# Kernel optimization log

Hardware: AMD Instinct MI355X
Metric: run time of the kernel (lower is better)

## Reference

```python
import jax, jax.numpy as jnp
import numpy as np

B, T, D = 2, 2048, 2048
H = 16
NOPE, ROPE = 128, 64
Q_HEAD = NOPE + ROPE            # 192
Q_LORA = H * Q_HEAD // 4        # 768
KV_RANK = 512
V_DIM = 128
EPS = 1e-6


def setup_inputs() -> dict:
    key = jax.random.key(0)
    ks = jax.random.split(key, 8)
    s = lambda k, shape: jax.random.normal(k, shape, dtype=jnp.float32) * (1.0 / np.sqrt(shape[0]))
    return {
        "hidden_states": jax.random.normal(ks[0], (B, T, D), dtype=jnp.float32),
        "positions": jnp.broadcast_to(jnp.arange(T, dtype=jnp.int64 if jax.config.jax_enable_x64 else jnp.int32), (B, T)),
        "w_qa": s(ks[1], (D, Q_LORA)),
        "g_qa": jnp.ones((Q_LORA,), jnp.float32),
        "w_qb": s(ks[2], (Q_LORA, H * Q_HEAD)),
        "w_kva": s(ks[3], (D, KV_RANK + ROPE)),
        "g_kva": jnp.ones((KV_RANK,), jnp.float32),
        "w_kvb": s(ks[4], (KV_RANK, H * (NOPE + V_DIM))),
        "w_o": s(ks[5], (H * V_DIM, D)),
    }


def _rms(x, g):
    return x * jax.lax.rsqrt(jnp.mean(x * x, axis=-1, keepdims=True) + EPS) * g


def _rotate_half(x):
    h = x.shape[-1] // 2
    return jnp.concatenate([-x[..., h:], x[..., :h]], axis=-1)


def _rope_tables(n):
    inv_freq = 1.0 / (10000.0 ** (jnp.arange(0, ROPE, 2, dtype=jnp.float32) / ROPE))
    freqs = jnp.arange(n, dtype=jnp.float32)[:, None] * inv_freq[None, :]
    emb = jnp.concatenate([freqs, freqs], axis=-1)  # [n, ROPE]
    return jnp.cos(emb), jnp.sin(emb)


def reference(hidden_states, positions, w_qa, g_qa, w_qb, w_kva, g_kva, w_kvb, w_o):
    Bq, Tq, _ = hidden_states.shape
    # Q: low-rank down-proj + RMSNorm + up-proj
    q = _rms(hidden_states @ w_qa, g_qa) @ w_qb
    q = q.reshape(Bq, Tq, H, Q_HEAD)
    q_nope, q_rope = q[..., :NOPE], q[..., NOPE:]
    # KV compression (prefill: no past cache, S == T)
    kvc = hidden_states @ w_kva
    new_c_kv = _rms(kvc[..., :KV_RANK], g_kva)     # [B,S,rank]
    new_k_rope = kvc[..., KV_RANK:]                # [B,S,ROPE]
    S = new_c_kv.shape[1]
    kv = (new_c_kv @ w_kvb).reshape(Bq, S, H, NOPE + V_DIM)
    k_nope, v = kv[..., :NOPE], kv[..., NOPE:]
    # Decoupled RoPE on the rope sub-dimension only
    cos_full, sin_full = _rope_tables(S)
    cos_q = cos_full[positions][:, :, None, :]     # [B,T,1,ROPE]
    sin_q = sin_full[positions][:, :, None, :]
    q_rope = q_rope * cos_q + _rotate_half(q_rope) * sin_q
    cos_k = cos_full[None, :, :]                   # [1,S,ROPE] (all_positions = arange(S))
    sin_k = sin_full[None, :, :]
    k_rope = new_k_rope * cos_k + _rotate_half(new_k_rope) * sin_k  # [B,S,ROPE], shared across heads
    # Assemble full q/k, attention
    q_full = jnp.concatenate([q_nope, q_rope], axis=-1).transpose(0, 2, 1, 3)  # [B,H,T,192]
    k_full = jnp.concatenate(
        [k_nope, jnp.broadcast_to(k_rope[:, :, None, :], (Bq, S, H, ROPE))], axis=-1
    ).transpose(0, 2, 1, 3)                                                     # [B,H,S,192]
    v = v.transpose(0, 2, 1, 3)                                                 # [B,H,S,Vd]
    scale = Q_HEAD ** -0.5
    attn = jnp.einsum("bhtd,bhsd->bhts", q_full, k_full) * scale
    row = jnp.arange(Tq)[:, None]
    col = jnp.arange(S)[None, :]
    attn = jnp.where(col > row + (S - Tq), -jnp.inf, attn)
    attn = jax.nn.softmax(attn, axis=-1)
    out = jnp.einsum("bhts,bhsd->bhtd", attn, v)
    out = out.transpose(0, 2, 1, 3).reshape(Bq, Tq, H * V_DIM)
    output = out @ w_o
    return output, new_c_kv, new_k_rope
```

## Files before the change

### kernel.cpp

```cpp
#include <hip/hip_runtime.h>
#include <stdint.h>

typedef unsigned short ushort_t;
typedef ushort_t u16x8 __attribute__((ext_vector_type(8)));
typedef short s16x8 __attribute__((ext_vector_type(8)));
typedef float f32x4 __attribute__((ext_vector_type(4)));

#define B_ 2
#define T_ 2048
#define D_ 2048
#define H_ 16
#define NOPE_ 128
#define ROPE_ 64
#define QHEAD_ 192
#define QLORA_ 768
#define KVRANK_ 512
#define VDIM_ 128
#define MROWS (B_*T_)
#define QKVW 1408

#define MAGIC_F32  0x3F800000u
#define MAGIC_BF16 0x3F803F80u

#define QK_SCALE2 0.10411754851533622f
#define DEFER_THR 11.5415603271117f

__device__ __forceinline__ float bf2f(ushort_t u) {
    return __uint_as_float(((uint32_t)u) << 16);
}
__device__ __forceinline__ ushort_t f2bf(float f) {
    uint32_t x = __float_as_uint(f);
    x += 0x7fffu + ((x >> 16) & 1u);
    return (ushort_t)(x >> 16);
}

__device__ __forceinline__ void async_ld16(const ushort_t* g, ushort_t* l) {
    __builtin_amdgcn_global_load_lds(
        (const __attribute__((address_space(1))) void*)g,
        (__attribute__((address_space(3))) void*)l, 16, 0, 0);
}

__device__ __forceinline__ void xcd_tile(int& m0, int& n0) {
    const int nx = gridDim.x;
    const int nwg = nx * gridDim.y;
    int lin = (int)blockIdx.y * nx + (int)blockIdx.x;
    lin = (lin & 7) * (nwg >> 3) + (lin >> 3);
    n0 = (lin % nx) * 128;
    m0 = (lin / nx) * 128;
}

__launch_bounds__(256)
__global__ void gemm_mfma(const ushort_t* __restrict__ A,
                          const ushort_t* __restrict__ BT,
                          float* __restrict__ C, int M, int N, int K) {
    __shared__ ushort_t As[128 * 32];
    __shared__ ushort_t Bs[128 * 32];

    const int tid = threadIdx.x;
    const int lane = tid & 63;
    const int n16 = lane & 15, quad = lane >> 4;
    int m0, n0;
    xcd_tile(m0, n0);
    const int w = tid >> 6;
    const int wm = (w & 1) * 64, wn = (w >> 1) * 64;

    f32x4 acc[4][4];
#pragma unroll
    for (int i = 0; i < 4; i++)
#pragma unroll
        for (int j = 0; j < 4; j++) acc[i][j] = (f32x4){0.f, 0.f, 0.f, 0.f};

    const int wbase = tid & ~63;
    for (int kt = 0; kt < K; kt += 32) {
        __syncthreads();
#pragma unroll
        for (int iss = 0; iss < 2; iss++) {
            const int chunk = iss * 256 + tid;
            const int row = chunk >> 2, col = (chunk & 3) * 8;
            const int lbase = (iss * 256 + wbase) * 8;
            async_ld16(A + (long)(m0 + row) * K + kt + col, &As[lbase]);
            async_ld16(BT + (long)(n0 + row) * K + kt + col, &Bs[lbase]);
        }
        __syncthreads();

        s16x8 af[4], bf[4];
#pragma unroll
        for (int i = 0; i < 4; i++) {
            af[i] = *(const s16x8*)&As[(wm + i * 16 + n16) * 32 + quad * 8];
            bf[i] = *(const s16x8*)&Bs[(wn + i * 16 + n16) * 32 + quad * 8];
        }
#pragma unroll
        for (int i = 0; i < 4; i++)
#pragma unroll
            for (int j = 0; j < 4; j++)
                acc[i][j] = __builtin_amdgcn_mfma_f32_16x16x32_bf16(af[i], bf[j], acc[i][j], 0, 0, 0);
    }

#pragma unroll
    for (int i = 0; i < 4; i++) {
        const long mrow = m0 + wm + i * 16 + quad * 4;
#pragma unroll
        for (int j = 0; j < 4; j++) {
            const int nc = n0 + wn + j * 16 + n16;
#pragma unroll
            for (int r = 0; r < 4; r++)
                C[(mrow + r) * N + nc] = acc[i][j][r];
        }
    }
}

__launch_bounds__(256)
__global__ void gemm_mfma_h(const ushort_t* __restrict__ A,
                            const ushort_t* __restrict__ BT,
                            ushort_t* __restrict__ C, int M, int N, int K) {
    __shared__ ushort_t As[128 * 32];
    __shared__ ushort_t Bs[128 * 32];

    const int tid = threadIdx.x;
    const int lane = tid & 63;
    const int n16 = lane & 15, quad = lane >> 4;
    int m0, n0;
    xcd_tile(m0, n0);
    const int w = tid >> 6;
    const int wm = (w & 1) * 64, wn = (w >> 1) * 64;

    f32x4 acc[4][4];
#pragma unroll
    for (int i = 0; i < 4; i++)
#pragma unroll
        for (int j = 0; j < 4; j++) acc[i][j] = (f32x4){0.f, 0.f, 0.f, 0.f};

    const int wbase = tid & ~63;
    for (int kt = 0; kt < K; kt += 32) {
        __syncthreads();
#pragma unroll
        for (int iss = 0; iss < 2; iss++) {
            const int chunk = iss * 256 + tid;
            const int row = chunk >> 2, col = (chunk & 3) * 8;
            const int lbase = (iss * 256 + wbase) * 8;
            async_ld16(A + (long)(m0 + row) * K + kt + col, &As[lbase]);
            async_ld16(BT + (long)(n0 + row) * K + kt + col, &Bs[lbase]);
        }
        __syncthreads();

        s16x8 af[4], bf[4];
#pragma unroll
        for (int i = 0; i < 4; i++) {
            af[i] = *(const s16x8*)&As[(wm + i * 16 + n16) * 32 + quad * 8];
            bf[i] = *(const s16x8*)&Bs[(wn + i * 16 + n16) * 32 + quad * 8];
        }
#pragma unroll
        for (int i = 0; i < 4; i++)
#pragma unroll
            for (int j = 0; j < 4; j++)
                acc[i][j] = __builtin_amdgcn_mfma_f32_16x16x32_bf16(af[i], bf[j], acc[i][j], 0, 0, 0);
    }

#pragma unroll
    for (int i = 0; i < 4; i++) {
        const long mrow = m0 + wm + i * 16 + quad * 4;
#pragma unroll
        for (int j = 0; j < 4; j++) {
            const int nc = n0 + wn + j * 16 + n16;
#pragma unroll
            for (int r = 0; r < 4; r++)
                C[(mrow + r) * N + nc] = f2bf(acc[i][j][r]);
        }
    }
}

__launch_bounds__(256)
__global__ void gemm_out_k(const uint32_t* __restrict__ probe,
                           const ushort_t* __restrict__ A,
                           const ushort_t* __restrict__ BT,
                           float* __restrict__ Cf, ushort_t* __restrict__ Ch,
                           int M, int N, int K) {
    __shared__ ushort_t As[128 * 32];
    __shared__ ushort_t Bs[128 * 32];

    const bool isf = (*probe == MAGIC_F32);
    const int tid = threadIdx.x;
    const int lane = tid & 63;
    const int n16 = lane & 15, quad = lane >> 4;
    int m0, n0;
    xcd_tile(m0, n0);
    const int w = tid >> 6;
    const int wm = (w & 1) * 64, wn = (w >> 1) * 64;

    f32x4 acc[4][4];
#pragma unroll
    for (int i = 0; i < 4; i++)
#pragma unroll
        for (int j = 0; j < 4; j++) acc[i][j] = (f32x4){0.f, 0.f, 0.f, 0.f};

    const int wbase = tid & ~63;
    for (int kt = 0; kt < K; kt += 32) {
        __syncthreads();
#pragma unroll
        for (int iss = 0; iss < 2; iss++) {
            const int chunk = iss * 256 + tid;
            const int row = chunk >> 2, col = (chunk & 3) * 8;
            const int lbase = (iss * 256 + wbase) * 8;
            async_ld16(A + (long)(m0 + row) * K + kt + col, &As[lbase]);
            async_ld16(BT + (long)(n0 + row) * K + kt + col, &Bs[lbase]);
        }
        __syncthreads();

        s16x8 af[4], bf[4];
#pragma unroll
        for (int i = 0; i < 4; i++) {
            af[i] = *(const s16x8*)&As[(wm + i * 16 + n16) * 32 + quad * 8];
            bf[i] = *(const s16x8*)&Bs[(wn + i * 16 + n16) * 32 + quad * 8];
        }
#pragma unroll
        for (int i = 0; i < 4; i++)
#pragma unroll
            for (int j = 0; j < 4; j++)
                acc[i][j] = __builtin_amdgcn_mfma_f32_16x16x32_bf16(af[i], bf[j], acc[i][j], 0, 0, 0);
    }

#pragma unroll
    for (int i = 0; i < 4; i++) {
        const long mrow = m0 + wm + i * 16 + quad * 4;
#pragma unroll
        for (int j = 0; j < 4; j++) {
            const int nc = n0 + wn + j * 16 + n16;
            if (isf) {
#pragma unroll
                for (int r = 0; r < 4; r++)
                    Cf[(mrow + r) * N + nc] = acc[i][j][r];
            } else {
#pragma unroll
                for (int r = 0; r < 4; r++)
                    Ch[(mrow + r) * N + nc] = f2bf(acc[i][j][r]);
            }
        }
    }
}

__launch_bounds__(256)
__global__ void gemm_kv_k(const ushort_t* __restrict__ A,
                          const ushort_t* __restrict__ BT,
                          ushort_t* __restrict__ kvK,
                          ushort_t* __restrict__ vTm,
                          int M, int N, int K) {
    __shared__ ushort_t As[128 * 32];
    __shared__ ushort_t Bs[128 * 32];

    const int tid = threadIdx.x;
    const int lane = tid & 63;
    const int n16 = lane & 15, quad = lane >> 4;
    int m0, n0;
    xcd_tile(m0, n0);
    const int w = tid >> 6;
    const int wm = (w & 1) * 64, wn = (w >> 1) * 64;

    f32x4 acc[4][4];
#pragma unroll
    for (int i = 0; i < 4; i++)
#pragma unroll
        for (int j = 0; j < 4; j++) acc[i][j] = (f32x4){0.f, 0.f, 0.f, 0.f};

    const int wbase = tid & ~63;
    for (int kt = 0; kt < K; kt += 32) {
        __syncthreads();
#pragma unroll
        for (int iss = 0; iss < 2; iss++) {
            const int chunk = iss * 256 + tid;
            const int row = chunk >> 2, col = (chunk & 3) * 8;
            const int lbase = (iss * 256 + wbase) * 8;
            async_ld16(A + (long)(m0 + row) * K + kt + col, &As[lbase]);
            async_ld16(BT + (long)(n0 + row) * K + kt + col, &Bs[lbase]);
        }
        __syncthreads();

        s16x8 af[4], bf[4];
#pragma unroll
        for (int i = 0; i < 4; i++) {
            af[i] = *(const s16x8*)&As[(wm + i * 16 + n16) * 32 + quad * 8];
            bf[i] = *(const s16x8*)&Bs[(wn + i * 16 + n16) * 32 + quad * 8];
        }
#pragma unroll
        for (int i = 0; i < 4; i++)
#pragma unroll
            for (int j = 0; j < 4; j++)
                acc[i][j] = __builtin_amdgcn_mfma_f32_16x16x32_bf16(af[i], bf[j], acc[i][j], 0, 0, 0);
    }

    const bool isV = (n0 & 128) != 0;
    if (!isV) {
#pragma unroll
        for (int i = 0; i < 4; i++) {
            const long mrowb = m0 + wm + i * 16 + quad * 4;
#pragma unroll
            for (int j = 0; j < 4; j++) {
                const int nc = n0 + wn + j * 16 + n16;
                const int hh = nc >> 8, dd = nc & 127;
#pragma unroll
                for (int r = 0; r < 4; r++)
                    kvK[(mrowb + r) * (H_ * NOPE_) + hh * NOPE_ + dd] = f2bf(acc[i][j][r]);
            }
        }
    } else {
        __syncthreads();
        ushort_t* tb = (w < 2) ? &As[w * 1152] : &Bs[(w - 2) * 1152];
        const int hh  = (n0 + wn) >> 8;
        const long bb = (long)((m0 + wm) >> 11);
        const int ssb = (m0 + wm) & (T_ - 1);
        const int ddb = (n0 + wn) & 127;
        const int ddr = lane >> 2;
        const int c0  = (lane & 3) * 16;
#pragma unroll
        for (int j = 0; j < 4; j++) {
#pragma unroll
            for (int i = 0; i < 4; i++)
#pragma unroll
                for (int r = 0; r < 4; r++)
                    tb[n16 * 72 + i * 16 + quad * 4 + r] = f2bf(acc[i][j][r]);
            u16x8 v0 = *(const u16x8*)&tb[ddr * 72 + c0];
            u16x8 v1 = *(const u16x8*)&tb[ddr * 72 + c0 + 8];
            ushort_t* dstp = vTm + ((bb * H_ + hh) * VDIM_ + ddb + j * 16 + ddr) * (long)T_ + ssb + c0;
            *(u16x8*)dstp = v0;
            *(u16x8*)(dstp + 8) = v1;
        }
    }
}

__launch_bounds__(256)
__global__ void cvt_trans_k(const uint32_t* __restrict__ probe,
                            const float* __restrict__ srcf,
                            const ushort_t* __restrict__ srch,
                            ushort_t* __restrict__ dst,
                            int K, int N, int NP, float scl) {
    const bool isf = (*probe == MAGIC_F32);
    __shared__ float tile[32][33];
    const int kb = blockIdx.y * 32, nb = blockIdx.x * 32;
    const int tx = threadIdx.x & 31, ty = threadIdx.x >> 5;
#pragma unroll
    for (int i = 0; i < 32; i += 8) {
        const int n = nb + tx;
        const long idx = (long)(kb + ty + i) * N + n;
        tile[ty + i][tx] = (n < N) ? (isf ? srcf[idx] : bf2f(srch[idx])) : 0.f;
    }
    __syncthreads();
#pragma unroll
    for (int i = 0; i < 32; i += 8) {
        const int n = nb + ty + i;
        if (n < NP) dst[(long)n * K + kb + tx] = f2bf(tile[tx][ty + i] * scl);
    }
}

__launch_bounds__(256)
__global__ void cvt_copy_k(const uint32_t* __restrict__ probe,
                           const float* __restrict__ srcf,
                           const ushort_t* __restrict__ srch,
                           ushort_t* __restrict__ dst, long n) {
    const bool isf = (*probe == MAGIC_F32);
    const long i = ((long)blockIdx.x * 256 + threadIdx.x) * 8;
    if (i + 8 <= n) {
        u16x8 o;
        if (isf) {
            float4 a = *(const float4*)(srcf + i);
            float4 b = *(const float4*)(srcf + i + 4);
            o[0]=f2bf(a.x); o[1]=f2bf(a.y); o[2]=f2bf(a.z); o[3]=f2bf(a.w);
            o[4]=f2bf(b.x); o[5]=f2bf(b.y); o[6]=f2bf(b.z); o[7]=f2bf(b.w);
        } else {
            o = *(const u16x8*)(srch + i);
        }
        *(u16x8*)(dst + i) = o;
    }
}

__launch_bounds__(256)
__global__ void rms12rope_k(const uint32_t* __restrict__ probe,
                            const float* __restrict__ qkv,
                            const float* __restrict__ g1f, const ushort_t* __restrict__ g1h,
                            const float* __restrict__ g2f, const ushort_t* __restrict__ g2h,
                            ushort_t* __restrict__ qln,
                            float* __restrict__ ockf, ushort_t* __restrict__ ockh,
                            ushort_t* __restrict__ ckv_i,
                            float* __restrict__ okrf, ushort_t* __restrict__ okrh,
                            ushort_t* __restrict__ krope_rot) {
    const bool isf = (*probe == MAGIC_F32);
    const int row = blockIdx.x;
    const int tid = threadIdx.x;
    const float* ir = qkv + (long)row * QKVW;

    float s1 = 0.f, s2 = 0.f;
    for (int c = tid; c < QLORA_; c += 256) { float x = ir[c]; s1 += x * x; }
    for (int c = tid; c < KVRANK_; c += 256) { float x = ir[QLORA_ + c]; s2 += x * x; }
    __shared__ float r1[256], r2[256];
    r1[tid] = s1; r2[tid] = s2;
    __syncthreads();
    for (int s = 128; s > 0; s >>= 1) {
        if (tid < s) { r1[tid] += r1[tid + s]; r2[tid] += r2[tid + s]; }
        __syncthreads();
    }
    const float inv1 = rsqrtf(r1[0] / (float)QLORA_ + 1e-6f);
    const float inv2 = rsqrtf(r2[0] / (float)KVRANK_ + 1e-6f);

    for (int c = tid; c < QLORA_; c += 256)
        qln[(long)row * QLORA_ + c] = f2bf(ir[c] * inv1 * (isf ? g1f[c] : bf2f(g1h[c])));
    for (int c = tid; c < KVRANK_; c += 256) {
        const float v = ir[QLORA_ + c] * inv2 * (isf ? g2f[c] : bf2f(g2h[c]));
        if (isf) ockf[(long)row * KVRANK_ + c] = v;
        else     ockh[(long)row * KVRANK_ + c] = f2bf(v);
        ckv_i[(long)row * KVRANK_ + c] = f2bf(v);
    }

    if (tid < 64) {
        const int lane = tid;
        const int t = row & (T_ - 1);
        const float x = ir[QLORA_ + KVRANK_ + lane];
        const float other = ir[QLORA_ + KVRANK_ + (lane ^ 32)];
        const int fi = lane & 31;
        const float inv_freq = exp2f((float)fi * (-13.287712379549449f / 32.f));
        const float ang = (float)t * inv_freq;
        float sn, cs;
        sincosf(ang, &sn, &cs);
        const float rot = (lane < 32) ? -other : other;
        if (isf) okrf[(long)row * ROPE_ + lane] = x;
        else     okrh[(long)row * ROPE_ + lane] = f2bf(x);
        krope_rot[(long)row * ROPE_ + lane] = f2bf(x * cs + rot * sn);
    }
}

#define BQ 64
#define BK 64
#define PSTR 68

__launch_bounds__(256, 2)
__global__ void attn_mfma_k(const ushort_t* __restrict__ q,
                            const ushort_t* __restrict__ kvK,
                            const ushort_t* __restrict__ vTm,
                            const ushort_t* __restrict__ krope,
                            ushort_t* __restrict__ attn_out) {
    __shared__ ushort_t ks[2][BK * 192];
    __shared__ ushort_t ps[4][16][PSTR];

    const int tid = threadIdx.x;
    const int w = tid >> 6, lane = tid & 63;
    const int n16 = lane & 15, quad = lane >> 4;

    const int L = (int)blockIdx.x;
    const int slot = L >> 3;
    const int bhg = slot >> 5;
    const int qts = slot & 31;
    const int bh = (L & 7) | (bhg << 3);
    const int qt = (bhg & 1) ? (31 - qts) : qts;
    const int h = bh & (H_ - 1), b = bh >> 4;

    const int q0 = qt * BQ;
    const int qw = q0 + w * 16;

    s16x8 qf[6];
    {
        const ushort_t* qrow = q + (long)(b * T_ + qw + n16) * (H_ * QHEAD_) + h * QHEAD_;
#pragma unroll
        for (int c = 0; c < 6; c++)
            qf[c] = *(const s16x8*)(qrow + c * 32 + quad * 8);
    }
    {
        const int t = qw + n16;
#pragma unroll
        for (int j = 0; j < 8; j++) {
            const int d = quad * 8 + j;
            const float inv_freq = exp2f((float)d * (-13.287712379549449f / 32.f));
            float sn, cs;
            sincosf((float)t * inv_freq, &sn, &cs);
            const float x0 = bf2f((ushort_t)qf[4][j]);
            const float x1 = bf2f((ushort_t)qf[5][j]);
            qf[4][j] = (short)f2bf(x0 * cs - x1 * sn);
            qf[5][j] = (short)f2bf(x1 * cs + x0 * sn);
        }
    }

    s16x8 kones;
#pragma unroll
    for (int j = 0; j < 8; j++) kones[j] = (short)0x3F80;

    f32x4 O[8];
#pragma unroll
    for (int f = 0; f < 8; f++) O[f] = (f32x4){0.f, 0.f, 0.f, 0.f};
    float mrow[4], lrow[4];
#pragma unroll
    for (int r = 0; r < 4; r++) { mrow[r] = -3.0e38f; lrow[r] = 0.f; }

    const int ntiles = qt + 1;

    const ushort_t* spb[6];  int sstr[6];
#pragma unroll
    for (int i = 0; i < 6; i++) {
        const int off = w * 6144 + i * 1024 + lane * 16;
        const int row = off / 384;
        const int c16 = (off % 384) >> 4;
        const int csrc = c16 ^ (row & 7);
        if (csrc < 16) {
            spb[i] = kvK + (long)(b * T_ + row) * (H_ * NOPE_) + h * NOPE_ + csrc * 8;
            sstr[i] = H_ * NOPE_;
        } else {
            spb[i] = krope + (long)(b * T_ + row) * ROPE_ + (csrc - 16) * 8;
            sstr[i] = ROPE_;
        }
    }

    const ushort_t* vbase = vTm + ((long)bh * VDIM_ + n16) * T_ + quad * 8;
    const int r7 = n16 & 7;

#pragma unroll
    for (int i = 0; i < 6; i++)
        async_ld16(spb[i], &ks[0][w * 3072 + i * 512]);

    int cur = 0;
    for (int kt = 0; kt < ntiles; kt++) {
        const int s0 = kt * BK;
        const int sn = (kt + 1 < ntiles ? kt + 1 : kt) * BK;

        s16x8 vb[2][8];
#pragma unroll
        for (int kc = 0; kc < 2; kc++)
#pragma unroll
            for (int vt = 0; vt < 8; vt++)
                vb[kc][vt] = *(const s16x8*)(vbase + (long)(vt * 16) * T_ + s0 + kc * 32);
        __builtin_amdgcn_sched_barrier(0);

        asm volatile("s_waitcnt vmcnt(16)" ::: "memory");
        __builtin_amdgcn_s_barrier();
        __builtin_amdgcn_sched_barrier(0);

#pragma unroll
        for (int i = 0; i < 6; i++)
            async_ld16(spb[i] + (long)sn * sstr[i], &ks[cur ^ 1][w * 3072 + i * 512]);
        __builtin_amdgcn_sched_barrier(0);

        const ushort_t* kb = &ks[cur][0];
        f32x4 Sc[4];
        __builtin_amdgcn_s_setprio(1);
#pragma unroll
        for (int st = 0; st < 4; st++) {
            Sc[st] = (f32x4){0.f, 0.f, 0.f, 0.f};
            const int row = st * 16 + n16;
            const int rbase = row * 192;
#pragma unroll
            for (int c = 0; c < 4; c++) {
                s16x8 bfr = *(const s16x8*)&kb[rbase + (((4 * c + quad) ^ r7) << 3)];
                Sc[st] = __builtin_amdgcn_mfma_f32_16x16x32_bf16(qf[c], bfr, Sc[st], 0, 0, 0);
            }
#pragma unroll
            for (int c2 = 0; c2 < 2; c2++) {
                s16x8 bfr = *(const s16x8*)&kb[rbase + (((16 + 4 * c2 + quad) ^ r7) << 3)];
                Sc[st] = __builtin_amdgcn_mfma_f32_16x16x32_bf16(qf[4 + c2], bfr, Sc[st], 0, 0, 0);
            }
        }
        __builtin_amdgcn_s_setprio(0);

        const bool diag = (s0 + BK > q0);
        float Sv[4][4];
#pragma unroll
        for (int st = 0; st < 4; st++) {
            const int sg = s0 + st * 16 + n16;
#pragma unroll
            for (int r = 0; r < 4; r++) {
                float v = Sc[st][r];
                if (diag && sg > qw + quad * 4 + r) v = -3.0e38f;
                Sv[st][r] = v;
            }
        }

        float rmx[4];
#pragma unroll
        for (int r = 0; r < 4; r++)
            rmx[r] = fmaxf(fmaxf(Sv[0][r], Sv[1][r]), fmaxf(Sv[2][r], Sv[3][r]));

        bool ok = true;
#pragma unroll
        for (int r = 0; r < 4; r++) ok = ok && (rmx[r] <= mrow[r] + DEFER_THR);
        if (!__all(ok)) {
            float mnew[4], alpha[4];
#pragma unroll
            for (int r = 0; r < 4; r++) {
                float mx = rmx[r];
#pragma unroll
                for (int off = 8; off > 0; off >>= 1)
                    mx = fmaxf(mx, __shfl_xor(mx, off, 64));
                mnew[r] = fmaxf(mrow[r], mx);
                alpha[r] = exp2f(mrow[r] - mnew[r]);
                mrow[r] = mnew[r];
                lrow[r] *= alpha[r];
            }
#pragma unroll
            for (int f = 0; f < 8; f++)
#pragma unroll
                for (int r = 0; r < 4; r++) O[f][r] *= alpha[r];
        }

#pragma unroll
        for (int st = 0; st < 4; st++)
#pragma unroll
            for (int r = 0; r < 4; r++)
                ps[w][quad * 4 + r][st * 16 + n16] = f2bf(exp2f(Sv[st][r] - mrow[r]));

        asm volatile("s_waitcnt vmcnt(6)" ::: "memory");
        __builtin_amdgcn_sched_barrier(0);

        f32x4 sacc = (f32x4){0.f, 0.f, 0.f, 0.f};
        __builtin_amdgcn_s_setprio(1);
#pragma unroll
        for (int kc = 0; kc < 2; kc++) {
            s16x8 afr = *(const s16x8*)&ps[w][n16][kc * 32 + quad * 8];
            sacc = __builtin_amdgcn_mfma_f32_16x16x32_bf16(afr, kones, sacc, 0, 0, 0);
#pragma unroll
            for (int vt = 0; vt < 8; vt++)
                O[vt] = __builtin_amdgcn_mfma_f32_16x16x32_bf16(afr, vb[kc][vt], O[vt], 0, 0, 0);
        }
        __builtin_amdgcn_s_setprio(0);
#pragma unroll
        for (int r = 0; r < 4; r++) lrow[r] += sacc[r];

        cur ^= 1;
    }

    float linv[4];
#pragma unroll
    for (int r = 0; r < 4; r++) linv[r] = 1.f / lrow[r];
    ushort_t* obase = attn_out + (long)(b * T_ + qw) * (H_ * VDIM_) + h * VDIM_;
#pragma unroll
    for (int vt = 0; vt < 8; vt++)
#pragma unroll
        for (int r = 0; r < 4; r++)
            obase[(long)(quad * 4 + r) * (H_ * VDIM_) + vt * 16 + n16] =
                f2bf(O[vt][r] * linv[r]);
}

extern "C" void kernel_launch(void* const* d_in, const int* in_sizes, int n_in,
                              void* d_out, int out_size, void* d_ws, size_t ws_size,
                              hipStream_t stream) {
    const uint32_t* probe = (const uint32_t*)d_in[3];

    char* ws = (char*)d_ws;
    ushort_t* q      = (ushort_t*)ws;
    ushort_t* hs_b   = (ushort_t*)ws;
    ushort_t* woT    = (ushort_t*)ws;
    ushort_t* kvK    = (ushort_t*)(ws + 25165824);
    ushort_t* vTm    = (ushort_t*)(ws + 41943040);
    float*    qkv    = (float*)(ws + 25165824);
    ushort_t* wqaT   = (ushort_t*)(ws + 48234496);
    ushort_t* wkvaT  = (ushort_t*)(ws + 51380224);
    ushort_t* wqbT   = (ushort_t*)(ws + 48234496);
    ushort_t* attn_i = (ushort_t*)(ws + 58720256);
    ushort_t* ckv_i  = (ushort_t*)(ws + 58720256);
    ushort_t* qln    = (ushort_t*)(ws + 62914560);
    ushort_t* wkvbT  = (ushort_t*)(ws + 69206016);
    ushort_t* krope  = (ushort_t*)(ws + 76283904 - 786432);

    const float* hs_f  = (const float*)d_in[0];
    const float* wqa_f = (const float*)d_in[2];
    const float* gqa_f = (const float*)d_in[3];
    const float* wqb_f = (const float*)d_in[4];
    const float* wkva_f= (const float*)d_in[5];
    const float* gkva_f= (const float*)d_in[6];
    const float* wkvb_f= (const float*)d_in[7];
    const float* wo_f  = (const float*)d_in[8];
    float* oy_f  = (float*)d_out;
    float* ock_f = oy_f + (long)MROWS * D_;
    float* okr_f = ock_f + (long)MROWS * KVRANK_;

    const ushort_t* hs_h  = (const ushort_t*)d_in[0];
    const ushort_t* wqa_h = (const ushort_t*)d_in[2];
    const ushort_t* gqa_h = (const ushort_t*)d_in[3];
    const ushort_t* wqb_h = (const ushort_t*)d_in[4];
    const ushort_t* wkva_h= (const ushort_t*)d_in[5];
    const ushort_t* gkva_h= (const ushort_t*)d_in[6];
    const ushort_t* wkvb_h= (const ushort_t*)d_in[7];
    const ushort_t* wo_h  = (const ushort_t*)d_in[8];
    ushort_t* oy_h  = (ushort_t*)d_out;
    ushort_t* ock_h = oy_h + (long)MROWS * D_;
    ushort_t* okr_h = ock_h + (long)MROWS * KVRANK_;

    const dim3 blk(256);

    cvt_copy_k<<<4096, blk, 0, stream>>>(probe, hs_f, hs_h, hs_b, (long)MROWS * D_);
    cvt_trans_k<<<dim3(24, 64), blk, 0, stream>>>(probe, wqa_f, wqa_h, wqaT, D_, QLORA_, QLORA_, 1.f);
    cvt_trans_k<<<dim3(20, 64), blk, 0, stream>>>(probe, wkva_f, wkva_h, wkvaT, D_, KVRANK_ + ROPE_, 640, 1.f);

    gemm_mfma<<<dim3(QKVW / 128, MROWS / 128), blk, 0, stream>>>(hs_b, wqaT, qkv, MROWS, QKVW, D_);

    rms12rope_k<<<MROWS, blk, 0, stream>>>(probe, qkv, gqa_f, gqa_h, gkva_f, gkva_h,
                                           qln, ock_f, ock_h, ckv_i, okr_f, okr_h, krope);

    cvt_trans_k<<<dim3(96, 24), blk, 0, stream>>>(probe, wqb_f, wqb_h, wqbT, QLORA_, H_ * QHEAD_, H_ * QHEAD_, QK_SCALE2);
    gemm_mfma_h<<<dim3((H_ * QHEAD_) / 128, MROWS / 128), blk, 0, stream>>>(qln, wqbT, q, MROWS, H_ * QHEAD_, QLORA_);

    cvt_trans_k<<<dim3(128, 16), blk, 0, stream>>>(probe, wkvb_f, wkvb_h, wkvbT, KVRANK_, H_ * 256, H_ * 256, 1.f);
    gemm_kv_k<<<dim3((H_ * 256) / 128, MROWS / 128), blk, 0, stream>>>(ckv_i, wkvbT, kvK, vTm, MROWS, H_ * 256, KVRANK_);

    attn_mfma_k<<<dim3(B_ * H_ * (T_ / BQ)), blk, 0, stream>>>(q, kvK, vTm, krope, attn_i);

    cvt_trans_k<<<dim3(64, 64), blk, 0, stream>>>(probe, wo_f, wo_h, woT, H_ * VDIM_, D_, D_, 1.f);
    gemm_out_k<<<dim3(D_ / 128, MROWS / 128), blk, 0, stream>>>(probe, attn_i, woT, oy_f, oy_h, MROWS, D_, H_ * VDIM_);
}
```

Measured before the change: 506.8 us.

## Widen GEMM K-tile to 64 and software-pipeline QK scores in attention

All four GEMM kernels now stage 64-wide K slices into shared memory instead of 32, halving the number of barrier pairs per output tile at the cost of doubled LDS use. The attention kernel is restructured so the QK score MFMAs for the next key tile are computed while the current tile's softmax and PV run, with K prefetch moved two tiles ahead. This is meant to hide LDS and global-load latency behind MFMA work, but it adds register pressure from the extra score accumulators.

```diff
diff --git a/kernel.cpp b/kernel.cpp
--- a/kernel.cpp
+++ b/kernel.cpp
@@ -49,12 +49,40 @@
     m0 = (lin / nx) * 128;
 }
 
+#define GEMM_STAGE64(As, Bs)                                                   \
+    __syncthreads();                                                           \
+    _Pragma("unroll")                                                          \
+    for (int iss = 0; iss < 4; iss++) {                                        \
+        const int chunk = iss * 256 + tid;                                     \
+        const int row = chunk >> 3, col = (chunk & 7) * 8;                     \
+        const int lbase = (iss * 256 + wbase) * 8;                             \
+        async_ld16(A + (long)(m0 + row) * K + kt + col, &As[lbase]);           \
+        async_ld16(BT + (long)(n0 + row) * K + kt + col, &Bs[lbase]);          \
+    }                                                                          \
+    __syncthreads();
+
+#define GEMM_MFMA64(As, Bs)                                                    \
+    _Pragma("unroll")                                                          \
+    for (int kc = 0; kc < 2; kc++) {                                           \
+        s16x8 af[4], bf[4];                                                    \
+        _Pragma("unroll")                                                      \
+        for (int i = 0; i < 4; i++) {                                          \
+            af[i] = *(const s16x8*)&As[(wm + i * 16 + n16) * 64 + kc * 32 + quad * 8]; \
+            bf[i] = *(const s16x8*)&Bs[(wn + i * 16 + n16) * 64 + kc * 32 + quad * 8]; \
+        }                                                                      \
+        _Pragma("unroll")                                                      \
+        for (int i = 0; i < 4; i++)                                            \
+            _Pragma("unroll")                                                  \
+            for (int j = 0; j < 4; j++)                                        \
+                acc[i][j] = __builtin_amdgcn_mfma_f32_16x16x32_bf16(af[i], bf[j], acc[i][j], 0, 0, 0); \
+    }
+
 __launch_bounds__(256)
 __global__ void gemm_mfma(const ushort_t* __restrict__ A,
                           const ushort_t* __restrict__ BT,
                           float* __restrict__ C, int M, int N, int K) {
-    __shared__ ushort_t As[128 * 32];
-    __shared__ ushort_t Bs[128 * 32];
+    __shared__ ushort_t As[128 * 64];
+    __shared__ ushort_t Bs[128 * 64];
 
     const int tid = threadIdx.x;
     const int lane = tid & 63;
@@ -71,29 +99,9 @@
         for (int j = 0; j < 4; j++) acc[i][j] = (f32x4){0.f, 0.f, 0.f, 0.f};
 
     const int wbase = tid & ~63;
-    for (int kt = 0; kt < K; kt += 32) {
-        __syncthreads();
-#pragma unroll
-        for (int iss = 0; iss < 2; iss++) {
-            const int chunk = iss * 256 + tid;
-            const int row = chunk >> 2, col = (chunk & 3) * 8;
-            const int lbase = (iss * 256 + wbase) * 8;
-            async_ld16(A + (long)(m0 + row) * K + kt + col, &As[lbase]);
-            async_ld16(BT + (long)(n0 + row) * K + kt + col, &Bs[lbase]);
-        }
-        __syncthreads();
-
-        s16x8 af[4], bf[4];
-#pragma unroll
-        for (int i = 0; i < 4; i++) {
-            af[i] = *(const s16x8*)&As[(wm + i * 16 + n16) * 32 + quad * 8];
-            bf[i] = *(const s16x8*)&Bs[(wn + i * 16 + n16) * 32 + quad * 8];
-        }
-#pragma unroll
-        for (int i = 0; i < 4; i++)
-#pragma unroll
-            for (int j = 0; j < 4; j++)
-                acc[i][j] = __builtin_amdgcn_mfma_f32_16x16x32_bf16(af[i], bf[j], acc[i][j], 0, 0, 0);
+    for (int kt = 0; kt < K; kt += 64) {
+        GEMM_STAGE64(As, Bs)
+        GEMM_MFMA64(As, Bs)
     }
 
 #pragma unroll
@@ -113,8 +121,8 @@
 __global__ void gemm_mfma_h(const ushort_t* __restrict__ A,
                             const ushort_t* __restrict__ BT,
                             ushort_t* __restrict__ C, int M, int N, int K) {
-    __shared__ ushort_t As[128 * 32];
-    __shared__ ushort_t Bs[128 * 32];
+    __shared__ ushort_t As[128 * 64];
+    __shared__ ushort_t Bs[128 * 64];
 
     const int tid = threadIdx.x;
     const int lane = tid & 63;
@@ -131,29 +139,9 @@
         for (int j = 0; j < 4; j++) acc[i][j] = (f32x4){0.f, 0.f, 0.f, 0.f};
 
     const int wbase = tid & ~63;
-    for (int kt = 0; kt < K; kt += 32) {
-        __syncthreads();
-#pragma unroll
-        for (int iss = 0; iss < 2; iss++) {
-            const int chunk = iss * 256 + tid;
-            const int row = chunk >> 2, col = (chunk & 3) * 8;
-            const int lbase = (iss * 256 + wbase) * 8;
-            async_ld16(A + (long)(m0 + row) * K + kt + col, &As[lbase]);
-            async_ld16(BT + (long)(n0 + row) * K + kt + col, &Bs[lbase]);
-        }
-        __syncthreads();
-
-        s16x8 af[4], bf[4];
-#pragma unroll
-        for (int i = 0; i < 4; i++) {
-            af[i] = *(const s16x8*)&As[(wm + i * 16 + n16) * 32 + quad * 8];
-            bf[i] = *(const s16x8*)&Bs[(wn + i * 16 + n16) * 32 + quad * 8];
-        }
-#pragma unroll
-        for (int i = 0; i < 4; i++)
-#pragma unroll
-            for (int j = 0; j < 4; j++)
-                acc[i][j] = __builtin_amdgcn_mfma_f32_16x16x32_bf16(af[i], bf[j], acc[i][j], 0, 0, 0);
+    for (int kt = 0; kt < K; kt += 64) {
+        GEMM_STAGE64(As, Bs)
+        GEMM_MFMA64(As, Bs)
     }
 
 #pragma unroll
@@ -175,8 +163,8 @@
                            const ushort_t* __restrict__ BT,
                            float* __restrict__ Cf, ushort_t* __restrict__ Ch,
                            int M, int N, int K) {
-    __shared__ ushort_t As[128 * 32];
-    __shared__ ushort_t Bs[128 * 32];
+    __shared__ ushort_t As[128 * 64];
+    __shared__ ushort_t Bs[128 * 64];
 
     const bool isf = (*probe == MAGIC_F32);
     const int tid = threadIdx.x;
@@ -194,29 +182,9 @@
         for (int j = 0; j < 4; j++) acc[i][j] = (f32x4){0.f, 0.f, 0.f, 0.f};
 
     const int wbase = tid & ~63;
-    for (int kt = 0; kt < K; kt += 32) {
-        __syncthreads();
-#pragma unroll
-        for (int iss = 0; iss < 2; iss++) {
-            const int chunk = iss * 256 + tid;
-            const int row = chunk >> 2, col = (chunk & 3) * 8;
-            const int lbase = (iss * 256 + wbase) * 8;
-            async_ld16(A + (long)(m0 + row) * K + kt + col, &As[lbase]);
-            async_ld16(BT + (long)(n0 + row) * K + kt + col, &Bs[lbase]);
-        }
-        __syncthreads();
-
-        s16x8 af[4], bf[4];
-#pragma unroll
-        for (int i = 0; i < 4; i++) {
-            af[i] = *(const s16x8*)&As[(wm + i * 16 + n16) * 32 + quad * 8];
-            bf[i] = *(const s16x8*)&Bs[(wn + i * 16 + n16) * 32 + quad * 8];
-        }
-#pragma unroll
-        for (int i = 0; i < 4; i++)
-#pragma unroll
-            for (int j = 0; j < 4; j++)
-                acc[i][j] = __builtin_amdgcn_mfma_f32_16x16x32_bf16(af[i], bf[j], acc[i][j], 0, 0, 0);
+    for (int kt = 0; kt < K; kt += 64) {
+        GEMM_STAGE64(As, Bs)
+        GEMM_MFMA64(As, Bs)
     }
 
 #pragma unroll
@@ -244,8 +212,8 @@
                           ushort_t* __restrict__ kvK,
                           ushort_t* __restrict__ vTm,
                           int M, int N, int K) {
-    __shared__ ushort_t As[128 * 32];
-    __shared__ ushort_t Bs[128 * 32];
+    __shared__ ushort_t As[128 * 64];
+    __shared__ ushort_t Bs[128 * 64];
 
     const int tid = threadIdx.x;
     const int lane = tid & 63;
@@ -262,29 +230,9 @@
         for (int j = 0; j < 4; j++) acc[i][j] = (f32x4){0.f, 0.f, 0.f, 0.f};
 
     const int wbase = tid & ~63;
-    for (int kt = 0; kt < K; kt += 32) {
-        __syncthreads();
-#pragma unroll
-        for (int iss = 0; iss < 2; iss++) {
-            const int chunk = iss * 256 + tid;
-            const int row = chunk >> 2, col = (chunk & 3) * 8;
-            const int lbase = (iss * 256 + wbase) * 8;
-            async_ld16(A + (long)(m0 + row) * K + kt + col, &As[lbase]);
-            async_ld16(BT + (long)(n0 + row) * K + kt + col, &Bs[lbase]);
-        }
-        __syncthreads();
-
-        s16x8 af[4], bf[4];
-#pragma unroll
-        for (int i = 0; i < 4; i++) {
-            af[i] = *(const s16x8*)&As[(wm + i * 16 + n16) * 32 + quad * 8];
-            bf[i] = *(const s16x8*)&Bs[(wn + i * 16 + n16) * 32 + quad * 8];
-        }
-#pragma unroll
-        for (int i = 0; i < 4; i++)
-#pragma unroll
-            for (int j = 0; j < 4; j++)
-                acc[i][j] = __builtin_amdgcn_mfma_f32_16x16x32_bf16(af[i], bf[j], acc[i][j], 0, 0, 0);
+    for (int kt = 0; kt < K; kt += 64) {
+        GEMM_STAGE64(As, Bs)
+        GEMM_MFMA64(As, Bs)
     }
 
     const bool isV = (n0 & 128) != 0;
@@ -507,14 +455,46 @@
     const ushort_t* vbase = vTm + ((long)bh * VDIM_ + n16) * T_ + quad * 8;
     const int r7 = n16 & 7;
 
+#define QK_TILE(dst, buf)                                                      \
+    {                                                                          \
+        const ushort_t* kb = &(buf)[0];                                        \
+        __builtin_amdgcn_s_setprio(1);                                         \
+        _Pragma("unroll")                                                      \
+        for (int st = 0; st < 4; st++) {                                       \
+            dst[st] = (f32x4){0.f, 0.f, 0.f, 0.f};                             \
+            const int krow = st * 16 + n16;                                    \
+            const int rbase = krow * 192;                                      \
+            _Pragma("unroll")                                                  \
+            for (int c = 0; c < 4; c++) {                                      \
+                s16x8 bfr = *(const s16x8*)&kb[rbase + (((4 * c + quad) ^ r7) << 3)]; \
+                dst[st] = __builtin_amdgcn_mfma_f32_16x16x32_bf16(qf[c], bfr, dst[st], 0, 0, 0); \
+            }                                                                  \
+            _Pragma("unroll")                                                  \
+            for (int c2 = 0; c2 < 2; c2++) {                                   \
+                s16x8 bfr = *(const s16x8*)&kb[rbase + (((16 + 4 * c2 + quad) ^ r7) << 3)]; \
+                dst[st] = __builtin_amdgcn_mfma_f32_16x16x32_bf16(qf[4 + c2], bfr, dst[st], 0, 0, 0); \
+            }                                                                  \
+        }                                                                      \
+        __builtin_amdgcn_s_setprio(0);                                         \
+    }
+
 #pragma unroll
     for (int i = 0; i < 6; i++)
         async_ld16(spb[i], &ks[0][w * 3072 + i * 512]);
-
-    int cur = 0;
+    asm volatile("s_waitcnt vmcnt(0)" ::: "memory");
+    __builtin_amdgcn_s_barrier();
+    {
+        const long sn1 = (1 < ntiles ? 1 : 0) * (long)BK;
+#pragma unroll
+        for (int i = 0; i < 6; i++)
+            async_ld16(spb[i] + sn1 * sstr[i], &ks[1][w * 3072 + i * 512]);
+    }
+    f32x4 Sc[4];
+    QK_TILE(Sc, ks[0])
+
     for (int kt = 0; kt < ntiles; kt++) {
         const int s0 = kt * BK;
-        const int sn = (kt + 1 < ntiles ? kt + 1 : kt) * BK;
+        const int cur = kt & 1;
 
         s16x8 vb[2][8];
 #pragma unroll
@@ -528,31 +508,16 @@
         __builtin_amdgcn_s_barrier();
         __builtin_amdgcn_sched_barrier(0);
 
-#pragma unroll
-        for (int i = 0; i < 6; i++)
-            async_ld16(spb[i] + (long)sn * sstr[i], &ks[cur ^ 1][w * 3072 + i * 512]);
+        {
+            const long sn2 = (long)(kt + 2 < ntiles ? kt + 2 : ntiles - 1) * BK;
+#pragma unroll
+            for (int i = 0; i < 6; i++)
+                async_ld16(spb[i] + sn2 * sstr[i], &ks[cur][w * 3072 + i * 512]);
+        }
         __builtin_amdgcn_sched_barrier(0);
 
-        const ushort_t* kb = &ks[cur][0];
-        f32x4 Sc[4];
-        __builtin_amdgcn_s_setprio(1);
-#pragma unroll
-        for (int st = 0; st < 4; st++) {
-            Sc[st] = (f32x4){0.f, 0.f, 0.f, 0.f};
-            const int row = st * 16 + n16;
-            const int rbase = row * 192;
-#pragma unroll
-            for (int c = 0; c < 4; c++) {
-                s16x8 bfr = *(const s16x8*)&kb[rbase + (((4 * c + quad) ^ r7) << 3)];
-                Sc[st] = __builtin_amdgcn_mfma_f32_16x16x32_bf16(qf[c], bfr, Sc[st], 0, 0, 0);
-            }
-#pragma unroll
-            for (int c2 = 0; c2 < 2; c2++) {
-                s16x8 bfr = *(const s16x8*)&kb[rbase + (((16 + 4 * c2 + quad) ^ r7) << 3)];
-                Sc[st] = __builtin_amdgcn_mfma_f32_16x16x32_bf16(qf[4 + c2], bfr, Sc[st], 0, 0, 0);
-            }
-        }
-        __builtin_amdgcn_s_setprio(0);
+        f32x4 Scn[4];
+        QK_TILE(Scn, ks[cur ^ 1])
 
         const bool diag = (s0 + BK > q0);
         float Sv[4][4];
@@ -617,7 +582,8 @@
 #pragma unroll
         for (int r = 0; r < 4; r++) lrow[r] += sacc[r];
 
-        cur ^= 1;
+#pragma unroll
+        for (int st = 0; st < 4; st++) Sc[st] = Scn[st];
     }
 
     float linv[4];
```

After: 524.4 us. 3.5% more time.
